# Kernel optimization log

Hardware: AMD Instinct MI355X
Metric: run time of the kernel (lower is better)

## Reference

```python
import jax, jax.numpy as jnp
import numpy as np

N = 100000       # nodes
DEG = 16         # fixed out/in degree used to build CSR
E = N * DEG      # edges
D_IN = 128       # in_feats
D_OUT = 256      # out_feats
K = 32           # maxk k_value


def _xavier_uniform(key, shape, gain):
    fan_out, fan_in = shape
    bound = gain * np.sqrt(6.0 / (fan_in + fan_out))
    return jax.random.uniform(key, shape, jnp.float32, -bound, bound)


def setup_inputs() -> dict:
    key = jax.random.key(0)
    ks = jax.random.split(key, 6)
    feat = jax.random.normal(ks[0], (N, D_IN), jnp.float32)
    topk_values = jax.random.uniform(ks[1], (N, K), jnp.float32)
    topk_indices = jax.random.randint(ks[2], (N, K), 0, D_IN).astype(jnp.int32)
    # CSR graph: fixed degree -> indptr is arange*DEG; random destinations
    indptr = (jnp.arange(N + 1) * DEG).astype(jnp.int32)
    indices = jax.random.randint(ks[3], (E,), 0, N).astype(jnp.int32)
    # set_graph_data: csr weight[e] = 1 / clamp(in_degree(dst), 1)
    in_deg = jax.ops.segment_sum(jnp.ones(E, jnp.float32), indices, num_segments=N)
    in_deg = jnp.maximum(in_deg, 1.0)
    csr_values = 1.0 / in_deg[indices]
    gain = np.sqrt(2.0)  # calculate_gain('relu')
    w_neigh = _xavier_uniform(ks[4], (D_OUT, D_IN), gain)
    w_self = _xavier_uniform(ks[5], (D_OUT, D_IN), gain)
    b_self = jnp.zeros((D_OUT,), jnp.float32)
    return {"feat": feat, "topk_values": topk_values, "csr_values": csr_values,
            "w_neigh": w_neigh, "w_self": w_self, "b_self": b_self,
            "topk_indices": topk_indices, "indptr": indptr, "indices": indices}


def reference(feat, topk_values, csr_values, w_neigh, w_self, b_self,
              topk_indices, indptr, indices):
    # Densify the k-sparse MaxK features: x[n, topk_indices[n, j]] = topk_values[n, j]
    x = jnp.zeros((N, D_IN), feat.dtype).at[
        jnp.arange(N)[:, None], topk_indices].add(topk_values)
    # Edge-weight-normalized SpMM over CSR: out[row] += w[e] * x[col[e]]
    row_ids = jnp.repeat(jnp.arange(N), jnp.diff(indptr), total_repeat_length=E)
    msgs = x[indices] * csr_values[:, None]          # [E, D_IN]
    agg = jax.ops.segment_sum(msgs, row_ids, num_segments=N)  # [N, D_IN]
    # lin_before_mp is False (in_feats <= out_feats): project after aggregation
    h_neigh = agg @ w_neigh.T                        # [N, D_OUT]
    rst = feat @ w_self.T + b_self + h_neigh         # fc_self(h_self) + h_neigh
    return rst
```

## Files before the change

kernel.cpp:

```cpp
#include <hip/hip_runtime.h>
#include <hip/hip_bf16.h>
#include <stdint.h>

#define N_NODES 100000
#define DEG 16
#define D_IN 128
#define D_OUT 256
#define K_TOP 32
#define K_CAT 256

typedef __attribute__((ext_vector_type(8))) short short8;
typedef __attribute__((ext_vector_type(4))) float floatx4;

__device__ __forceinline__ unsigned pack_bf16_rne(float f) {
    union { float f; unsigned u; } c; c.f = f;
    unsigned u = c.u;
    return (u + 0x7fffu + ((u >> 16) & 1u)) >> 16;
}
__device__ __forceinline__ float bf16lo_to_f(unsigned lo16) {
    union { unsigned u; float f; } c; c.u = lo16 << 16; return c.f;
}

typedef __attribute__((address_space(1))) void as1_void;
typedef __attribute__((address_space(3))) void as3_void;
__device__ __forceinline__ void gload_lds16(const void* g, void* l) {
    __builtin_amdgcn_global_load_lds((as1_void*)g, (as3_void*)l, 16, 0, 0);
}

__global__ __launch_bounds__(256) void k_packw(const float* __restrict__ w_self,
                                               const float* __restrict__ w_neigh,
                                               unsigned short* __restrict__ bmat) {
    int o = blockIdx.x;
    int k = threadIdx.x;
    float v = (k < D_IN) ? w_self[o * D_IN + k] : w_neigh[o * D_IN + (k - D_IN)];
    bmat[o * K_CAT + k] = (unsigned short)pack_bf16_rne(v);
}

#define DROWS 64
__global__ __launch_bounds__(256) void k_densify(const float* __restrict__ topk_v,
                                                 const int* __restrict__ topk_i,
                                                 const float* __restrict__ feat,
                                                 unsigned short* __restrict__ xbf,
                                                 unsigned short* __restrict__ abf) {
    __shared__ float sx[DROWS * D_IN];
    const int t = threadIdx.x;
    const int row0 = blockIdx.x * DROWS;

    #pragma unroll
    for (int p = 0; p < 8; ++p)
        *(floatx4*)&sx[(t + p * 256) * 4] = (floatx4){0.f, 0.f, 0.f, 0.f};
    __syncthreads();

    const size_t tbase = (size_t)row0 * K_TOP;
    #pragma unroll
    for (int p = 0; p < 8; ++p) {
        int q = t + p * 256;
        int r = q >> 5;
        if (row0 + r < N_NODES) {
            int   ci = topk_i[tbase + q];
            float cv = topk_v[tbase + q];
            atomicAdd(&sx[r * D_IN + ci], cv);
        }
    }
    __syncthreads();

    #pragma unroll
    for (int p = 0; p < 16; ++p) {
        int d = t + p * 256;
        int r = d >> 6;
        int c2 = (d & 63) * 2;
        if (row0 + r < N_NODES) {
            float2 v = *(const float2*)&sx[r * D_IN + c2];
            ((unsigned*)(xbf + (size_t)(row0 + r) * D_IN))[d & 63] =
                pack_bf16_rne(v.x) | (pack_bf16_rne(v.y) << 16);
        }
    }

    #pragma unroll
    for (int p = 0; p < 8; ++p) {
        int q = t + p * 256;
        int r = q >> 5;
        int c4 = (q & 31) * 4;
        if (row0 + r < N_NODES) {
            float4 f = *(const float4*)(feat + (size_t)(row0 + r) * D_IN + c4);
            uint2 pk;
            pk.x = pack_bf16_rne(f.x) | (pack_bf16_rne(f.y) << 16);
            pk.y = pack_bf16_rne(f.z) | (pack_bf16_rne(f.w) << 16);
            ((uint2*)(abf + (size_t)(row0 + r) * K_CAT))[q & 31] = pk;
        }
    }
}

__global__ __launch_bounds__(256) void k_spmm(const float* __restrict__ csr_w,
                                              const int* __restrict__ col_idx,
                                              const unsigned short* __restrict__ xbf,
                                              unsigned short* __restrict__ abf) {
    const int lane = threadIdx.x & 63;
    const int wave = threadIdx.x >> 6;
    const int ql   = lane & 15;
    const int row  = blockIdx.x * 16 + wave * 4 + (lane >> 4);
    const int qb   = lane & 48;

    int   c = col_idx[row * DEG + ql];
    float w = csr_w[row * DEG + ql];

    uint4 vv[DEG];
    #pragma unroll
    for (int e = 0; e < DEG; ++e) {
        int col = __shfl(c, qb | e);
        vv[e] = *(const uint4*)(xbf + (size_t)col * D_IN + ql * 8);
    }
    float a[8] = {0.f, 0.f, 0.f, 0.f, 0.f, 0.f, 0.f, 0.f};
    #pragma unroll
    for (int e = 0; e < DEG; ++e) {
        float we = __shfl(w, qb | e);
        uint4 v = vv[e];
        a[0] += we * bf16lo_to_f(v.x & 0xffffu);
        a[1] += we * bf16lo_to_f(v.x >> 16);
        a[2] += we * bf16lo_to_f(v.y & 0xffffu);
        a[3] += we * bf16lo_to_f(v.y >> 16);
        a[4] += we * bf16lo_to_f(v.z & 0xffffu);
        a[5] += we * bf16lo_to_f(v.z >> 16);
        a[6] += we * bf16lo_to_f(v.w & 0xffffu);
        a[7] += we * bf16lo_to_f(v.w >> 16);
    }
    uint4 pk;
    pk.x = pack_bf16_rne(a[0]) | (pack_bf16_rne(a[1]) << 16);
    pk.y = pack_bf16_rne(a[2]) | (pack_bf16_rne(a[3]) << 16);
    pk.z = pack_bf16_rne(a[4]) | (pack_bf16_rne(a[5]) << 16);
    pk.w = pack_bf16_rne(a[6]) | (pack_bf16_rne(a[7]) << 16);
    *(uint4*)(abf + (size_t)row * K_CAT + D_IN + ql * 8) = pk;
}

#define BM 128
#define BN 128
#define BK 32
#define NT (K_CAT / BK)

__global__ __launch_bounds__(256, 4) void k_gemm(const unsigned short* __restrict__ abf,
                                                 const unsigned short* __restrict__ bmat,
                                                 const float* __restrict__ bias,
                                                 float* __restrict__ out) {
    __shared__ __align__(16) unsigned short As[2][BM * BK];
    __shared__ __align__(16) unsigned short Bs[2][BN * BK];
    const int lane = threadIdx.x & 63, wave = threadIdx.x >> 6;
    const int wr = wave >> 1, wc = wave & 1;
    const int l16 = lane & 15, quad = lane >> 4;
    const int rt = blockIdx.x >> 1, ct = blockIdx.x & 1;
    const int row0 = rt * BM, n0 = ct * BN;

    const int sr = wave * 32 + (lane >> 2);
    const int sc = (lane & 3) * 8;
    int arow0 = row0 + sr;      if (arow0 >= N_NODES) arow0 = N_NODES - 1;
    int arow1 = row0 + sr + 16; if (arow1 >= N_NODES) arow1 = N_NODES - 1;
    const int brow0 = n0 + sr, brow1 = n0 + sr + 16;
    const unsigned short* ga0 = abf  + (size_t)arow0 * K_CAT + sc;
    const unsigned short* ga1 = abf  + (size_t)arow1 * K_CAT + sc;
    const unsigned short* gb0 = bmat + (size_t)brow0 * K_CAT + sc;
    const unsigned short* gb1 = bmat + (size_t)brow1 * K_CAT + sc;

#define STAGE(buf, kt) do {                                                  \
        gload_lds16(ga0 + (kt), &As[buf][(wave * 32)      * BK]);            \
        gload_lds16(ga1 + (kt), &As[buf][(wave * 32 + 16) * BK]);            \
        gload_lds16(gb0 + (kt), &Bs[buf][(wave * 32)      * BK]);            \
        gload_lds16(gb1 + (kt), &Bs[buf][(wave * 32 + 16) * BK]);            \
    } while (0)

    floatx4 acc[4][4];
    #pragma unroll
    for (int i = 0; i < 4; ++i)
        #pragma unroll
        for (int j = 0; j < 4; ++j)
            acc[i][j] = (floatx4){0.f, 0.f, 0.f, 0.f};

    STAGE(0, 0);
    __syncthreads();

    for (int t8 = 0; t8 < NT; ++t8) {
        const int cur = t8 & 1;
        if (t8 + 1 < NT) STAGE(cur ^ 1, (t8 + 1) * BK);

        short8 afr[4], bfr[4];
        #pragma unroll
        for (int i = 0; i < 4; ++i)
            afr[i] = *(const short8*)&As[cur][(wr * 64 + i * 16 + l16) * BK + quad * 8];
        #pragma unroll
        for (int j = 0; j < 4; ++j)
            bfr[j] = *(const short8*)&Bs[cur][(wc * 64 + j * 16 + l16) * BK + quad * 8];

        #pragma unroll
        for (int i = 0; i < 4; ++i)
            #pragma unroll
            for (int j = 0; j < 4; ++j)
                acc[i][j] = __builtin_amdgcn_mfma_f32_16x16x32_bf16(bfr[j], afr[i], acc[i][j], 0, 0, 0);

        if (t8 + 1 < NT) __syncthreads();
    }

    #pragma unroll
    for (int j = 0; j < 4; ++j) {
        const int cg = n0 + wc * 64 + j * 16 + quad * 4;
        const float4 bv = *(const float4*)&bias[cg];
        #pragma unroll
        for (int i = 0; i < 4; ++i) {
            const int gr = row0 + wr * 64 + i * 16 + l16;
            if (gr < N_NODES) {
                float4 v;
                v.x = acc[i][j][0] + bv.x;
                v.y = acc[i][j][1] + bv.y;
                v.z = acc[i][j][2] + bv.z;
                v.w = acc[i][j][3] + bv.w;
                *(float4*)(out + (size_t)gr * D_OUT + cg) = v;
            }
        }
    }
#undef STAGE
}

extern "C" void kernel_launch(void* const* d_in, const int* in_sizes, int n_in,
                              void* d_out, int out_size, void* d_ws, size_t ws_size,
                              hipStream_t stream) {
    const float* feat    = (const float*)d_in[0];
    const float* topk_v  = (const float*)d_in[1];
    const float* csr_w   = (const float*)d_in[2];
    const float* w_neigh = (const float*)d_in[3];
    const float* w_self  = (const float*)d_in[4];
    const float* b_self  = (const float*)d_in[5];
    const int*   topk_i  = (const int*)d_in[6];
    const int*   indices = (const int*)d_in[8];
    float* out = (float*)d_out;

    unsigned short* xbf  = (unsigned short*)d_ws;
    unsigned short* abf  = xbf + (size_t)N_NODES * D_IN;
    unsigned short* bmat = abf + (size_t)N_NODES * K_CAT;

    k_packw<<<dim3(256), dim3(256), 0, stream>>>(w_self, w_neigh, bmat);
    k_densify<<<dim3((N_NODES + DROWS - 1) / DROWS), dim3(256), 0, stream>>>(topk_v, topk_i, feat, xbf, abf);
    k_spmm<<<dim3(N_NODES / 16), dim3(256), 0, stream>>>(csr_w, indices, xbf, abf);
    k_gemm<<<dim3(2 * ((N_NODES + BM - 1) / BM)), dim3(256), 0, stream>>>(abf, bmat, b_self, out);
}
```

Measured before the change: 302.5 us.

## Fuse SpMM aggregation into GEMM via LDS-resident aggregated tile

Removes the separate SpMM kernel. Each 128-row GEMM block now gathers neighbor features itself, aggregates them into a swizzled LDS buffer, and reads them as the second half of the K dimension. The block also widens to 512 threads covering all 256 output columns, so each row is processed once instead of twice. This saves the global write and re-read of the aggregated activations and one launch. The cost is larger LDS use, lower occupancy, and a gather phase that stalls the GEMM pipeline at block start.

```diff
diff --git a/kernel.cpp b/kernel.cpp
--- a/kernel.cpp
+++ b/kernel.cpp
@@ -41,7 +41,7 @@
                                                  const int* __restrict__ topk_i,
                                                  const float* __restrict__ feat,
                                                  unsigned short* __restrict__ xbf,
-                                                 unsigned short* __restrict__ abf) {
+                                                 unsigned short* __restrict__ fbf) {
     __shared__ float sx[DROWS * D_IN];
     const int t = threadIdx.x;
     const int row0 = blockIdx.x * DROWS;
@@ -86,86 +86,87 @@
             uint2 pk;
             pk.x = pack_bf16_rne(f.x) | (pack_bf16_rne(f.y) << 16);
             pk.y = pack_bf16_rne(f.z) | (pack_bf16_rne(f.w) << 16);
-            ((uint2*)(abf + (size_t)(row0 + r) * K_CAT))[q & 31] = pk;
-        }
-    }
-}
-
-__global__ __launch_bounds__(256) void k_spmm(const float* __restrict__ csr_w,
-                                              const int* __restrict__ col_idx,
-                                              const unsigned short* __restrict__ xbf,
-                                              unsigned short* __restrict__ abf) {
-    const int lane = threadIdx.x & 63;
-    const int wave = threadIdx.x >> 6;
-    const int ql   = lane & 15;
-    const int row  = blockIdx.x * 16 + wave * 4 + (lane >> 4);
-    const int qb   = lane & 48;
-
-    int   c = col_idx[row * DEG + ql];
-    float w = csr_w[row * DEG + ql];
-
-    uint4 vv[DEG];
-    #pragma unroll
-    for (int e = 0; e < DEG; ++e) {
-        int col = __shfl(c, qb | e);
-        vv[e] = *(const uint4*)(xbf + (size_t)col * D_IN + ql * 8);
-    }
-    float a[8] = {0.f, 0.f, 0.f, 0.f, 0.f, 0.f, 0.f, 0.f};
-    #pragma unroll
-    for (int e = 0; e < DEG; ++e) {
-        float we = __shfl(w, qb | e);
-        uint4 v = vv[e];
-        a[0] += we * bf16lo_to_f(v.x & 0xffffu);
-        a[1] += we * bf16lo_to_f(v.x >> 16);
-        a[2] += we * bf16lo_to_f(v.y & 0xffffu);
-        a[3] += we * bf16lo_to_f(v.y >> 16);
-        a[4] += we * bf16lo_to_f(v.z & 0xffffu);
-        a[5] += we * bf16lo_to_f(v.z >> 16);
-        a[6] += we * bf16lo_to_f(v.w & 0xffffu);
-        a[7] += we * bf16lo_to_f(v.w >> 16);
-    }
-    uint4 pk;
-    pk.x = pack_bf16_rne(a[0]) | (pack_bf16_rne(a[1]) << 16);
-    pk.y = pack_bf16_rne(a[2]) | (pack_bf16_rne(a[3]) << 16);
-    pk.z = pack_bf16_rne(a[4]) | (pack_bf16_rne(a[5]) << 16);
-    pk.w = pack_bf16_rne(a[6]) | (pack_bf16_rne(a[7]) << 16);
-    *(uint4*)(abf + (size_t)row * K_CAT + D_IN + ql * 8) = pk;
+            ((uint2*)(fbf + (size_t)(row0 + r) * D_IN))[q & 31] = pk;
+        }
+    }
 }
 
 #define BM 128
-#define BN 128
+#define BN 256
 #define BK 32
-#define NT (K_CAT / BK)
-
-__global__ __launch_bounds__(256, 4) void k_gemm(const unsigned short* __restrict__ abf,
-                                                 const unsigned short* __restrict__ bmat,
-                                                 const float* __restrict__ bias,
-                                                 float* __restrict__ out) {
+#define NTA 4
+#define NT  8
+
+__global__ __launch_bounds__(512, 2) void k_fused(const float* __restrict__ csr_w,
+                                                  const int* __restrict__ col_idx,
+                                                  const unsigned short* __restrict__ xbf,
+                                                  const unsigned short* __restrict__ fbf,
+                                                  const unsigned short* __restrict__ bmat,
+                                                  const float* __restrict__ bias,
+                                                  float* __restrict__ out) {
+    __shared__ __align__(16) unsigned short Agg[BM * 128];
     __shared__ __align__(16) unsigned short As[2][BM * BK];
     __shared__ __align__(16) unsigned short Bs[2][BN * BK];
-    const int lane = threadIdx.x & 63, wave = threadIdx.x >> 6;
-    const int wr = wave >> 1, wc = wave & 1;
-    const int l16 = lane & 15, quad = lane >> 4;
-    const int rt = blockIdx.x >> 1, ct = blockIdx.x & 1;
-    const int row0 = rt * BM, n0 = ct * BN;
-
-    const int sr = wave * 32 + (lane >> 2);
-    const int sc = (lane & 3) * 8;
-    int arow0 = row0 + sr;      if (arow0 >= N_NODES) arow0 = N_NODES - 1;
-    int arow1 = row0 + sr + 16; if (arow1 >= N_NODES) arow1 = N_NODES - 1;
-    const int brow0 = n0 + sr, brow1 = n0 + sr + 16;
-    const unsigned short* ga0 = abf  + (size_t)arow0 * K_CAT + sc;
-    const unsigned short* ga1 = abf  + (size_t)arow1 * K_CAT + sc;
-    const unsigned short* gb0 = bmat + (size_t)brow0 * K_CAT + sc;
-    const unsigned short* gb1 = bmat + (size_t)brow1 * K_CAT + sc;
-
-#define STAGE(buf, kt) do {                                                  \
-        gload_lds16(ga0 + (kt), &As[buf][(wave * 32)      * BK]);            \
-        gload_lds16(ga1 + (kt), &As[buf][(wave * 32 + 16) * BK]);            \
-        gload_lds16(gb0 + (kt), &Bs[buf][(wave * 32)      * BK]);            \
-        gload_lds16(gb1 + (kt), &Bs[buf][(wave * 32 + 16) * BK]);            \
+    const int t    = threadIdx.x;
+    const int lane = t & 63, wave = t >> 6;
+    const int l16  = lane & 15, quad = lane >> 4;
+    const int row0 = blockIdx.x * BM;
+
+    const int a_r = wave * 16 + (lane >> 2);
+    const int a_c = (lane & 3) * 8;
+    int a_gr = row0 + a_r; if (a_gr >= N_NODES) a_gr = N_NODES - 1;
+    const unsigned short* gA  = fbf  + (size_t)a_gr * D_IN + a_c;
+    const unsigned short* gB0 = bmat + (size_t)a_r        * K_CAT + a_c;
+    const unsigned short* gB1 = bmat + (size_t)(a_r + 128) * K_CAT + a_c;
+
+#define STAGE_A(buf, tt) gload_lds16(gA + (tt) * BK, &As[buf][wave * 16 * BK])
+#define STAGE_B(buf, tt) do {                                                 \
+        gload_lds16(gB0 + (tt) * BK, &Bs[buf][(wave * 16)       * BK]);       \
+        gload_lds16(gB1 + (tt) * BK, &Bs[buf][(wave * 16 + 128) * BK]);       \
     } while (0)
 
+    STAGE_A(0, 0);
+    STAGE_B(0, 0);
+
+    const int ql = lane & 15, qb = lane & 48;
+    #pragma unroll 1
+    for (int p = 0; p < 4; ++p) {
+        const int r  = p * 32 + wave * 4 + (lane >> 4);
+        const int gr = row0 + r;
+        int   c = 0; float w = 0.f;
+        if (gr < N_NODES) {
+            c = col_idx[gr * DEG + ql];
+            w = csr_w [gr * DEG + ql];
+        }
+        uint4 vv[DEG];
+        #pragma unroll
+        for (int e = 0; e < DEG; ++e) {
+            int col = __shfl(c, qb | e);
+            vv[e] = *(const uint4*)(xbf + (size_t)col * D_IN + ql * 8);
+        }
+        float a[8] = {0.f, 0.f, 0.f, 0.f, 0.f, 0.f, 0.f, 0.f};
+        #pragma unroll
+        for (int e = 0; e < DEG; ++e) {
+            float we = __shfl(w, qb | e);
+            uint4 v = vv[e];
+            a[0] += we * bf16lo_to_f(v.x & 0xffffu);
+            a[1] += we * bf16lo_to_f(v.x >> 16);
+            a[2] += we * bf16lo_to_f(v.y & 0xffffu);
+            a[3] += we * bf16lo_to_f(v.y >> 16);
+            a[4] += we * bf16lo_to_f(v.z & 0xffffu);
+            a[5] += we * bf16lo_to_f(v.z >> 16);
+            a[6] += we * bf16lo_to_f(v.w & 0xffffu);
+            a[7] += we * bf16lo_to_f(v.w >> 16);
+        }
+        uint4 pk;
+        pk.x = pack_bf16_rne(a[0]) | (pack_bf16_rne(a[1]) << 16);
+        pk.y = pack_bf16_rne(a[2]) | (pack_bf16_rne(a[3]) << 16);
+        pk.z = pack_bf16_rne(a[4]) | (pack_bf16_rne(a[5]) << 16);
+        pk.w = pack_bf16_rne(a[6]) | (pack_bf16_rne(a[7]) << 16);
+        *(uint4*)&Agg[r * 128 + ((ql * 8) ^ ((r & 7) << 3))] = pk;
+    }
+
+    const int wr = wave >> 2, wc = wave & 3;
     floatx4 acc[4][4];
     #pragma unroll
     for (int i = 0; i < 4; ++i)
@@ -173,17 +174,27 @@
         for (int j = 0; j < 4; ++j)
             acc[i][j] = (floatx4){0.f, 0.f, 0.f, 0.f};
 
-    STAGE(0, 0);
     __syncthreads();
 
-    for (int t8 = 0; t8 < NT; ++t8) {
-        const int cur = t8 & 1;
-        if (t8 + 1 < NT) STAGE(cur ^ 1, (t8 + 1) * BK);
+    #pragma unroll
+    for (int tt = 0; tt < NT; ++tt) {
+        const int cur = tt & 1;
+        if (tt + 1 < NTA) STAGE_A(cur ^ 1, tt + 1);
+        if (tt + 1 < NT)  STAGE_B(cur ^ 1, tt + 1);
 
         short8 afr[4], bfr[4];
-        #pragma unroll
-        for (int i = 0; i < 4; ++i)
-            afr[i] = *(const short8*)&As[cur][(wr * 64 + i * 16 + l16) * BK + quad * 8];
+        if (tt < NTA) {
+            #pragma unroll
+            for (int i = 0; i < 4; ++i)
+                afr[i] = *(const short8*)&As[cur][(wr * 64 + i * 16 + l16) * BK + quad * 8];
+        } else {
+            const int c0 = (tt - NTA) * 32 + quad * 8;
+            #pragma unroll
+            for (int i = 0; i < 4; ++i) {
+                const int m = wr * 64 + i * 16 + l16;
+                afr[i] = *(const short8*)&Agg[m * 128 + (c0 ^ ((m & 7) << 3))];
+            }
+        }
         #pragma unroll
         for (int j = 0; j < 4; ++j)
             bfr[j] = *(const short8*)&Bs[cur][(wc * 64 + j * 16 + l16) * BK + quad * 8];
@@ -194,12 +205,12 @@
             for (int j = 0; j < 4; ++j)
                 acc[i][j] = __builtin_amdgcn_mfma_f32_16x16x32_bf16(bfr[j], afr[i], acc[i][j], 0, 0, 0);
 
-        if (t8 + 1 < NT) __syncthreads();
+        if (tt + 1 < NT) __syncthreads();
     }
 
     #pragma unroll
     for (int j = 0; j < 4; ++j) {
-        const int cg = n0 + wc * 64 + j * 16 + quad * 4;
+        const int cg = wc * 64 + j * 16 + quad * 4;
         const float4 bv = *(const float4*)&bias[cg];
         #pragma unroll
         for (int i = 0; i < 4; ++i) {
@@ -214,7 +225,8 @@
             }
         }
     }
-#undef STAGE
+#undef STAGE_A
+#undef STAGE_B
 }
 
 extern "C" void kernel_launch(void* const* d_in, const int* in_sizes, int n_in,
@@ -231,11 +243,10 @@
     float* out = (float*)d_out;
 
     unsigned short* xbf  = (unsigned short*)d_ws;
-    unsigned short* abf  = xbf + (size_t)N_NODES * D_IN;
-    unsigned short* bmat = abf + (size_t)N_NODES * K_CAT;
+    unsigned short* fbf  = xbf + (size_t)N_NODES * D_IN;
+    unsigned short* bmat = fbf + (size_t)N_NODES * D_IN;
 
     k_packw<<<dim3(256), dim3(256), 0, stream>>>(w_self, w_neigh, bmat);
-    k_densify<<<dim3((N_NODES + DROWS - 1) / DROWS), dim3(256), 0, stream>>>(topk_v, topk_i, feat, xbf, abf);
-    k_spmm<<<dim3(N_NODES / 16), dim3(256), 0, stream>>>(csr_w, indices, xbf, abf);
-    k_gemm<<<dim3(2 * ((N_NODES + BM - 1) / BM)), dim3(256), 0, stream>>>(abf, bmat, b_self, out);
-}
+    k_densify<<<dim3((N_NODES + DROWS - 1) / DROWS), dim3(256), 0, stream>>>(topk_v, topk_i, feat, xbf, fbf);
+    k_fused<<<dim3((N_NODES + BM - 1) / BM), dim3(512), 0, stream>>>(csr_w, indices, xbf, fbf, bmat, b_self, out);
+}
```

After: 296.2 us. 1.02x faster.
